# Kernel optimization log

Measured on AMD Instinct MI355X. Metric: run time of the kernel, lower is better.

## Reference

```python
import jax, jax.numpy as jnp
import numpy as np

BINS = 32
MAX_DIST = 128
EMB = 1024
DQ = 64
DV = 64
H = 16
B = 8
L = 1024


def _t5_bucket_table():
    # matches: clamp(n,max=m) + (log(clamp(n,min=m)-m+1)*(bins-1-m)/log(max_distance-m+1)).long()
    n = np.arange(MAX_DIST + 1)
    m = BINS // 2
    idx = np.minimum(n, m) + (
        np.log(np.maximum(n, m) - m + 1) * (BINS - 1 - m) / np.log(MAX_DIST - m + 1)
    ).astype(np.int64)
    return jnp.asarray(idx)


def setup_inputs() -> dict:
    key = jax.random.key(0)
    ks = jax.random.split(key, 8)
    s = 0.02
    return {
        "x": jax.random.normal(ks[0], (B, L, EMB), dtype=jnp.float32),
        "qk_w": jax.random.normal(ks[1], (2 * DQ * H, EMB), dtype=jnp.float32) * s,
        "qk_b": jnp.zeros((2 * DQ * H,), dtype=jnp.float32),
        "v_w": jax.random.normal(ks[2], (DV * H, EMB), dtype=jnp.float32) * s,
        "v_b": jnp.zeros((DV * H,), dtype=jnp.float32),
        "out_w": jax.random.normal(ks[3], (EMB, DV * H), dtype=jnp.float32) * s,
        "out_b": jnp.zeros((EMB,), dtype=jnp.float32),
        "bias": jax.random.normal(ks[4], (BINS, H), dtype=jnp.float32) * s,  # causal -> bins rows
    }


def reference(x, qk_w, qk_b, v_w, v_b, out_w, out_b, bias):
    # projections
    qk = (x @ qk_w.T + qk_b).reshape(B, L, H, 2 * DQ).transpose(0, 2, 1, 3)  # [B,H,L,2DQ]
    q, k = qk[..., :DQ], qk[..., DQ:]
    v = (x @ v_w.T + v_b).reshape(B, L, H, DV).transpose(0, 2, 1, 3)  # [B,H,L,DV]

    # T5 relative-position bias (causal): gather per (i-j) distance bucket
    idx_tab = _t5_bucket_table()
    shifts = jnp.arange(L)[:, None] - jnp.arange(L)[None, :]  # [L,L], i - j
    bins_idx = idx_tab[jnp.clip(jnp.abs(shifts), 0, MAX_DIST)]  # [L,L]
    bmat = bias[bins_idx].transpose(2, 0, 1)  # [H,L,L]
    bmat = jnp.where(shifts < 0, -jnp.inf, bmat)  # causal mask (j > i)

    scale = 1.0 / np.sqrt(DQ).astype(np.float32)
    scores = jnp.einsum("bhid,bhjd->bhij", q, k) * scale + bmat  # [B,H,L,L]
    attn = jax.nn.softmax(scores, axis=-1)
    out = jnp.einsum("bhij,bhjd->bhid", attn, v)  # [B,H,L,DV]
    out = out.transpose(0, 2, 1, 3).reshape(B, L, H * DV)
    return out @ out_w.T + out_b
```

## Files before the change

kernel.cpp:

```cpp
#include <hip/hip_runtime.h>
#include <cmath>


typedef _Float16 f16x8 __attribute__((ext_vector_type(8)));
typedef _Float16 f16x4 __attribute__((ext_vector_type(4)));
typedef float    f32x4 __attribute__((ext_vector_type(4)));

#define NEG_INF (-__builtin_inff())
#define LOG2E 1.4426950408889634f

#if __has_builtin(__builtin_amdgcn_exp2f)
#define EXP2(x) __builtin_amdgcn_exp2f(x)
#else
#define EXP2(x) exp2f(x)
#endif

__device__ __forceinline__ void gl_lds16(const void* g, void* l) {
  __builtin_amdgcn_global_load_lds(
      (__attribute__((address_space(1))) void*)g,
      (__attribute__((address_space(3))) void*)l,
      16, 0, 0);
}

__device__ __forceinline__ f32x4 mfma32(f16x8 a, f16x8 b, f32x4 c) {
  return __builtin_amdgcn_mfma_f32_16x16x32_f16(a, b, c, 0, 0, 0);
}
__device__ __forceinline__ f32x4 mfma16(f16x4 a, f16x4 b, f32x4 c) {
  return __builtin_amdgcn_mfma_f32_16x16x16f16(a, b, c, 0, 0, 0);
}

typedef __attribute__((address_space(3))) _Float16* lds_f16p;

#define DSR(d, a, o) \
  asm volatile("ds_read_b128 %0, %1 offset:" o : "=v"(d) : "v"(a))

__global__ void cvt4_kernel(const float* __restrict__ x,
                            const float* __restrict__ w1,
                            const float* __restrict__ w2,
                            const float* __restrict__ w3,
                            _Float16* __restrict__ ox, _Float16* __restrict__ o1,
                            _Float16* __restrict__ o2, _Float16* __restrict__ o3) {
  const int bid = blockIdx.x;
  const float* src;
  _Float16* dst;
  int idx;
  if (bid < 8192) {
    src = x; dst = ox; idx = bid * 256 + threadIdx.x;
  } else if (bid < 10240) {
    src = w1; dst = o1; idx = (bid - 8192) * 256 + threadIdx.x;
  } else if (bid < 11264) {
    src = w2; dst = o2; idx = (bid - 10240) * 256 + threadIdx.x;
  } else {
    src = w3; dst = o3; idx = (bid - 11264) * 256 + threadIdx.x;
  }
  float4 v = reinterpret_cast<const float4*>(src)[idx];
  f16x4 o;
  o[0] = (_Float16)v.x; o[1] = (_Float16)v.y;
  o[2] = (_Float16)v.z; o[3] = (_Float16)v.w;
  reinterpret_cast<f16x4*>(dst)[idx] = o;
}

#define GEMM_VM8 asm volatile("s_waitcnt vmcnt(8)" ::: "memory")
#define GEMM_VM4 asm volatile("s_waitcnt vmcnt(4)" ::: "memory")
#define GEMM_VM0 asm volatile("s_waitcnt vmcnt(0)" ::: "memory")
#define GEMM_BAR __builtin_amdgcn_s_barrier()

#define GEMM_STAGE(buf, kk)                                        \
  do {                                                             \
    gl_lds16(pA0 + (kk), &lds[(buf)*4096 + wofs]);                 \
    gl_lds16(pA1 + (kk), &lds[(buf)*4096 + 2048 + wofs]);          \
    gl_lds16(pB0 + (kk), &lds[12288 + (buf)*4096 + wofs]);         \
    gl_lds16(pB1 + (kk), &lds[12288 + (buf)*4096 + 2048 + wofs]);  \
  } while (0)

#define GEMM_COMPUTE(aB, bB)                             \
  do {                                                   \
    f16x8 af0, af1, af2, af3, bf0, bf1, bf2, bf3;        \
    DSR(af0, aB, "0");                                   \
    DSR(bf0, bB, "0");                                   \
    DSR(af1, aB, "1024");                                \
    DSR(bf1, bB, "1024");                                \
    DSR(af2, aB, "2048");                                \
    DSR(bf2, bB, "2048");                                \
    DSR(af3, aB, "3072");                                \
    DSR(bf3, bB, "3072");                                \
    asm volatile("s_waitcnt lgkmcnt(4)" ::: "memory");   \
    __builtin_amdgcn_sched_barrier(0);                   \
    __builtin_amdgcn_s_setprio(1);                       \
    acc[0][0] = mfma32(af0, bf0, acc[0][0]);             \
    acc[0][1] = mfma32(af0, bf1, acc[0][1]);             \
    acc[1][0] = mfma32(af1, bf0, acc[1][0]);             \
    acc[1][1] = mfma32(af1, bf1, acc[1][1]);             \
    asm volatile("s_waitcnt lgkmcnt(0)" ::: "memory");   \
    __builtin_amdgcn_sched_barrier(0);                   \
    acc[0][2] = mfma32(af0, bf2, acc[0][2]);             \
    acc[0][3] = mfma32(af0, bf3, acc[0][3]);             \
    acc[1][2] = mfma32(af1, bf2, acc[1][2]);             \
    acc[1][3] = mfma32(af1, bf3, acc[1][3]);             \
    acc[2][0] = mfma32(af2, bf0, acc[2][0]);             \
    acc[2][1] = mfma32(af2, bf1, acc[2][1]);             \
    acc[2][2] = mfma32(af2, bf2, acc[2][2]);             \
    acc[2][3] = mfma32(af2, bf3, acc[2][3]);             \
    acc[3][0] = mfma32(af3, bf0, acc[3][0]);             \
    acc[3][1] = mfma32(af3, bf1, acc[3][1]);             \
    acc[3][2] = mfma32(af3, bf2, acc[3][2]);             \
    acc[3][3] = mfma32(af3, bf3, acc[3][3]);             \
    __builtin_amdgcn_s_setprio(0);                       \
  } while (0)

template <int MODE>
__global__ __launch_bounds__(256, 3) void gemm_kernel(
    const _Float16* __restrict__ A, const _Float16* __restrict__ Bm,
    int M, int N, int K,
    const float* __restrict__ bias_q, const float* __restrict__ bias_v,
    _Float16* __restrict__ qkbuf, _Float16* __restrict__ vtbuf,
    const float* __restrict__ bias_o, float* __restrict__ outf) {
  __shared__ __align__(16) _Float16 lds[6 * 4096];
  const int t = threadIdx.x;
  const int w = t >> 6;
  const int lane = t & 63;
  const int lq = lane & 15, lg = lane >> 4;
  const int wr = w >> 1, wc = w & 1;
  const int m0 = blockIdx.y * 128, n0 = blockIdx.x * 128;

  const int stc = ((t & 3) ^ ((t >> 3) & 3)) * 8;
  const _Float16* pA0 = A + (size_t)(m0 + (t >> 2)) * K + stc;
  const _Float16* pA1 = pA0 + (size_t)64 * K;
  const _Float16* pB0 = Bm + (size_t)(n0 + (t >> 2)) * K + stc;
  const _Float16* pB1 = pB0 + (size_t)64 * K;
  const int wofs = w * 512;

  const int xsw = (lq >> 1) & 3;
  const uint32_t base = (uint32_t)(uintptr_t)(lds_f16p)&lds[0];
  const uint32_t aB0 =
      base + (uint32_t)((wr * 64 + lq) * 64 + ((lg ^ xsw) << 4));
  const uint32_t aB1 = aB0 + 8192;
  const uint32_t aB2 = aB0 + 16384;
  const uint32_t bB0 =
      base + 24576 + (uint32_t)((wc * 64 + lq) * 64 + ((lg ^ xsw) << 4));
  const uint32_t bB1 = bB0 + 8192;
  const uint32_t bB2 = bB0 + 16384;

  f32x4 acc[4][4];
#pragma unroll
  for (int mi = 0; mi < 4; ++mi)
#pragma unroll
    for (int ni = 0; ni < 4; ++ni) acc[mi][ni] = (f32x4){0.f, 0.f, 0.f, 0.f};

  GEMM_STAGE(0, 0);
  GEMM_STAGE(1, 32);
  for (int kt = 0; kt + 160 <= K; kt += 96) {
    GEMM_STAGE(2, kt + 64);
    GEMM_VM8;
    GEMM_BAR;
    GEMM_COMPUTE(aB0, bB0);
    GEMM_BAR;
    GEMM_STAGE(0, kt + 96);
    GEMM_VM8;
    GEMM_BAR;
    GEMM_COMPUTE(aB1, bB1);
    GEMM_BAR;
    GEMM_STAGE(1, kt + 128);
    GEMM_VM8;
    GEMM_BAR;
    GEMM_COMPUTE(aB2, bB2);
    GEMM_BAR;
  }
  GEMM_VM4;
  GEMM_BAR;
  GEMM_COMPUTE(aB0, bB0);
  GEMM_BAR;
  GEMM_VM0;
  GEMM_BAR;
  GEMM_COMPUTE(aB1, bB1);

  if (MODE == 0) {
    GEMM_BAR;
    _Float16* T = &lds[0];
    const bool isqk = (n0 < 2048);
    const int bb = m0 >> 10, ii0 = m0 & 1023;
    if (isqk) {
#pragma unroll
      for (int mi = 0; mi < 4; ++mi)
#pragma unroll
        for (int ni = 0; ni < 4; ++ni) {
          const int col = wc * 64 + ni * 16 + lq;
          const float bq = bias_q[n0 + col];
#pragma unroll
          for (int r = 0; r < 4; ++r) {
            const int row = wr * 64 + mi * 16 + lg * 4 + r;
            T[row * 136 + col] = (_Float16)(acc[mi][ni][r] + bq);
          }
        }
      __syncthreads();
      const int hh = n0 >> 7;
      _Float16* gb = qkbuf + ((size_t)((bb * 16 + hh) * 1024 + ii0)) * 128;
      const int row = t >> 1, half = t & 1;
      const int so = row * 136 + half * 64;
      const int go = row * 128 + half * 64;
#pragma unroll
      for (int j = 0; j < 8; ++j)
        *(f16x8*)(gb + go + j * 8) = *(const f16x8*)&T[so + j * 8];
    } else {
      const int nn0 = n0 - 2048;
#pragma unroll
      for (int mi = 0; mi < 4; ++mi)
#pragma unroll
        for (int ni = 0; ni < 4; ++ni) {
          const int col = wc * 64 + ni * 16 + lq;
          const float bv = bias_v[nn0 + col];
          const int row0 = wr * 64 + mi * 16 + lg * 4;
          f16x4 p;
#pragma unroll
          for (int r = 0; r < 4; ++r) p[r] = (_Float16)(acc[mi][ni][r] + bv);
          *(f16x4*)&T[col * 136 + row0] = p;
        }
      __syncthreads();
      const int c = t >> 1, half = t & 1;
      const int nn = nn0 + c;
      const int hh = nn >> 6, dv = nn & 63;
      _Float16* gb = vtbuf + ((size_t)((bb * 16 + hh) * 64 + dv)) * 1024 +
                     ii0 + half * 64;
      const int so = c * 136 + half * 64;
#pragma unroll
      for (int j = 0; j < 8; ++j)
        *(f16x8*)(gb + j * 8) = *(const f16x8*)&T[so + j * 8];
    }
  } else {
#pragma unroll
    for (int mi = 0; mi < 4; ++mi)
#pragma unroll
      for (int ni = 0; ni < 4; ++ni)
#pragma unroll
        for (int r = 0; r < 4; ++r) {
          const int mg = m0 + wr * 64 + mi * 16 + lg * 4 + r;
          const int ng = n0 + wc * 64 + ni * 16 + lq;
          outf[(size_t)mg * N + ng] = acc[mi][ni][r] + bias_o[ng];
        }
  }
}

__device__ __forceinline__ void stage_kv(const _Float16* __restrict__ kb,
                                         const _Float16* __restrict__ vtb,
                                         int j0, _Float16* kl, _Float16* vl,
                                         int t) {
  const int r0 = t >> 3, c0 = t & 7;
  const int r1 = r0 + 32;
  const int kc0 = c0 ^ (r0 & 7), kc1 = c0 ^ (r1 & 7);
  gl_lds16(kb + (size_t)(j0 + r0) * 128 + kc0 * 8, kl + t * 8);
  gl_lds16(kb + (size_t)(j0 + r1) * 128 + kc1 * 8, kl + (t + 256) * 8);
  gl_lds16(vtb + (size_t)r0 * 1024 + j0 + kc0 * 8, vl + t * 8);
  gl_lds16(vtb + (size_t)r1 * 1024 + j0 + kc1 * 8, vl + (t + 256) * 8);
}

__device__ __forceinline__ void softmax16(f32x4 (&st)[4], f16x4 (&ph)[4],
                                          int qi, int j0, bool far,
                                          const float* __restrict__ tab,
                                          float t128, int lg4, float& m_run,
                                          float& l_part, f32x4 (&oacc)[4]) {
  float xs[16];
  float lmax = NEG_INF;
  if (far) {
#pragma unroll
    for (int js = 0; js < 4; ++js)
#pragma unroll
      for (int r = 0; r < 4; ++r) {
        const float xv = fmaf(st[js][r], 0.125f * LOG2E, t128);
        xs[js * 4 + r] = xv;
        lmax = fmaxf(lmax, xv);
      }
  } else {
#pragma unroll
    for (int js = 0; js < 4; ++js)
#pragma unroll
      for (int r = 0; r < 4; ++r) {
        const int jj = j0 + js * 16 + lg4 + r;
        const int dd = qi - jj;
        const int idx = dd < 0 ? 0 : (dd > 128 ? 128 : dd);
        const float xv =
            (dd < 0) ? NEG_INF : fmaf(st[js][r], 0.125f * LOG2E, tab[idx]);
        xs[js * 4 + r] = xv;
        lmax = fmaxf(lmax, xv);
      }
  }
  if (__any(lmax > m_run + 8.0f)) {
    float tmax = fmaxf(lmax, __shfl_xor(lmax, 16));
    tmax = fmaxf(tmax, __shfl_xor(tmax, 32));
    const float m_new = fmaxf(m_run, tmax);
    const float sf = EXP2(m_run - m_new);
    m_run = m_new;
    l_part *= sf;
    f32x4 sfv;
#pragma unroll
    for (int r = 0; r < 4; ++r) sfv[r] = __shfl(sf, lg4 + r);
#pragma unroll
    for (int db = 0; db < 4; ++db) oacc[db] *= sfv;
  }
  float ls = 0.f;
#pragma unroll
  for (int js = 0; js < 4; ++js)
#pragma unroll
    for (int r = 0; r < 4; ++r) {
      const float p = EXP2(xs[js * 4 + r] - m_run);
      ls += p;
      ph[js][r] = (_Float16)p;
    }
  l_part += ls;
}

__global__ __launch_bounds__(256, 4) void attn_kernel(
    const _Float16* __restrict__ qk,
    const _Float16* __restrict__ vt,
    const float* __restrict__ bias,
    _Float16* __restrict__ ao) {
  __shared__ __align__(16) _Float16 kls[2][64 * 64];
  __shared__ __align__(16) _Float16 vls[2][64 * 64];
  __shared__ float tab[132];
  const int t = threadIdx.x;
  const int bid = blockIdx.x;
  const int bh = (bid & 7) * 16 + (bid >> 6);
  const int b4 = (bid >> 3) & 7;
  const int h = bh & 15, b = bh >> 4;
  if (t < 129) {
    const int bucket =
        (t <= 16) ? t : 16 + (int)(log((double)(t - 15)) * 15.0 / log(113.0));
    tab[t] = bias[bucket * 16 + h] * LOG2E;
  }

  const int w = t >> 6, lane = t & 63;
  const int lq = lane & 15, lg = lane >> 4;
  const int lg4 = lg * 4, lg8 = lg * 8;
  const int tA = b4, tB = 15 - b4;
  const int q0A = tA * 64 + w * 16, q0B = tB * 64 + w * 16;
  const int qA = q0A + lq, qB = q0B + lq;
  const _Float16* qkb = qk + (size_t)bh * 1024 * 128;
  const _Float16* kb = qkb + 64;
  const _Float16* vtb = vt + (size_t)bh * 64 * 1024;

  const f16x8 qfA0 = *(const f16x8*)&qkb[qA * 128 + lg8];
  const f16x8 qfA1 = *(const f16x8*)&qkb[qA * 128 + 32 + lg8];
  const f16x8 qfB0 = *(const f16x8*)&qkb[qB * 128 + lg8];
  const f16x8 qfB1 = *(const f16x8*)&qkb[qB * 128 + 32 + lg8];

  f32x4 oA[4], oB[4];
#pragma unroll
  for (int db = 0; db < 4; ++db) {
    oA[db] = (f32x4){0.f, 0.f, 0.f, 0.f};
    oB[db] = (f32x4){0.f, 0.f, 0.f, 0.f};
  }
  float mA = NEG_INF, lAp = 0.f, mB = NEG_INF, lBp = 0.f;

  stage_kv(kb, vtb, 0, kls[0], vls[0], t);
  __syncthreads();
  const float t128 = tab[128];
  const int krsw = lq & 7;
  const int vsw = (lq & 7) << 1;
  int cur = 0;

  for (int jt = 0; jt <= tB; ++jt) {
    const int j0 = jt * 64;
    if (jt < tB) stage_kv(kb, vtb, j0 + 64, kls[cur ^ 1], vls[cur ^ 1], t);
    const bool aact = (jt <= tA);
    const _Float16* kbf = kls[cur];
    const _Float16* vbf = vls[cur];

    f32x4 stA[4], stB[4];
#pragma unroll
    for (int js = 0; js < 4; ++js) {
      const int rowb = (js * 16 + lq) * 64;
      const f16x8 kf0 = *(const f16x8*)&kbf[rowb + ((lg ^ krsw) << 3)];
      const f16x8 kf1 = *(const f16x8*)&kbf[rowb + (((lg + 4) ^ krsw) << 3)];
      if (aact) {
        stA[js] = mfma32(kf0, qfA0, (f32x4){0.f, 0.f, 0.f, 0.f});
        stA[js] = mfma32(kf1, qfA1, stA[js]);
      }
      stB[js] = mfma32(kf0, qfB0, (f32x4){0.f, 0.f, 0.f, 0.f});
      stB[js] = mfma32(kf1, qfB1, stB[js]);
    }

    f16x4 phA[4], phB[4];
    if (aact)
      softmax16(stA, phA, qA, j0, q0A - j0 >= 192, tab, t128, lg4, mA, lAp,
                oA);
    softmax16(stB, phB, qB, j0, q0B - j0 >= 192, tab, t128, lg4, mB, lBp, oB);

#pragma unroll
    for (int js = 0; js < 4; ++js)
#pragma unroll
      for (int db = 0; db < 4; ++db) {
        const f16x4 vf = *(const f16x4*)&vbf[(db * 16 + lq) * 64 +
                                             ((((js << 2) + lg) ^ vsw) << 2)];
        if (aact) oA[db] = mfma16(phA[js], vf, oA[db]);
        oB[db] = mfma16(phB[js], vf, oB[db]);
      }

    __syncthreads();
    cur ^= 1;
  }

  _Float16* aob = ao + ((size_t)b * 1024) * 1024 + h * 64;
  {
    float lt = lAp + __shfl_xor(lAp, 16);
    lt += __shfl_xor(lt, 32);
    f32x4 linv;
#pragma unroll
    for (int r = 0; r < 4; ++r) linv[r] = 1.0f / __shfl(lt, lg4 + r);
#pragma unroll
    for (int db = 0; db < 4; ++db)
#pragma unroll
      for (int r = 0; r < 4; ++r)
        aob[(size_t)(q0A + lg4 + r) * 1024 + db * 16 + lq] =
            (_Float16)(oA[db][r] * linv[r]);
  }
  {
    float lt = lBp + __shfl_xor(lBp, 16);
    lt += __shfl_xor(lt, 32);
    f32x4 linv;
#pragma unroll
    for (int r = 0; r < 4; ++r) linv[r] = 1.0f / __shfl(lt, lg4 + r);
#pragma unroll
    for (int db = 0; db < 4; ++db)
#pragma unroll
      for (int r = 0; r < 4; ++r)
        aob[(size_t)(q0B + lg4 + r) * 1024 + db * 16 + lq] =
            (_Float16)(oB[db][r] * linv[r]);
  }
}

extern "C" void kernel_launch(void* const* d_in, const int* in_sizes, int n_in,
                              void* d_out, int out_size, void* d_ws,
                              size_t ws_size, hipStream_t stream) {
  const float* x = (const float*)d_in[0];
  const float* qk_w = (const float*)d_in[1];
  const float* qk_b = (const float*)d_in[2];
  const float* v_w = (const float*)d_in[3];
  const float* v_b = (const float*)d_in[4];
  const float* out_w = (const float*)d_in[5];
  const float* out_b = (const float*)d_in[6];
  const float* bias = (const float*)d_in[7];
  float* out = (float*)d_out;

  _Float16* xb = (_Float16*)d_ws;
  _Float16* wb = xb + (size_t)8388608;
  _Float16* owb = wb + (size_t)3145728;
  _Float16* qkbuf = owb + (size_t)1048576;
  _Float16* vtbuf = qkbuf + (size_t)16777216;
  _Float16* ao = vtbuf + (size_t)8388608;

  cvt4_kernel<<<12288, 256, 0, stream>>>(x, qk_w, v_w, out_w, xb, wb,
                                         wb + 2097152, owb);

  gemm_kernel<0><<<dim3(24, 64), 256, 0, stream>>>(
      xb, wb, 8192, 3072, 1024, qk_b, v_b, qkbuf, vtbuf, nullptr, nullptr);

  attn_kernel<<<1024, 256, 0, stream>>>(qkbuf, vtbuf, bias, ao);

  gemm_kernel<1><<<dim3(8, 64), 256, 0, stream>>>(
      ao, owb, 8192, 1024, 1024, nullptr, nullptr, nullptr, nullptr, out_b, out);
}
```

Measured before the change: 157.6 us.

## Share K/V tiles across two query-tile pairs with 512-thread attention blocks

The attention kernel now uses 512-thread blocks, each processing two pairs of causal query tiles. The two pairs share every staged K/V tile, which halves the global-to-LDS staging per query and the block count. Rows whose causal range ends early are masked per wave with a new bact flag, so those waves sit idle on later iterations. Separately, the GEMM main loop is restructured to use a single wait-plus-barrier per stage instead of two barriers, and its loop bound is hardcoded to K=1024.

```diff
diff --git a/kernel.cpp b/kernel.cpp
--- a/kernel.cpp
+++ b/kernel.cpp
@@ -60,7 +60,6 @@
   reinterpret_cast<f16x4*>(dst)[idx] = o;
 }
 
-#define GEMM_VM8 asm volatile("s_waitcnt vmcnt(8)" ::: "memory")
 #define GEMM_VM4 asm volatile("s_waitcnt vmcnt(4)" ::: "memory")
 #define GEMM_VM0 asm volatile("s_waitcnt vmcnt(0)" ::: "memory")
 #define GEMM_BAR __builtin_amdgcn_s_barrier()
@@ -149,27 +148,23 @@
 
   GEMM_STAGE(0, 0);
   GEMM_STAGE(1, 32);
-  for (int kt = 0; kt + 160 <= K; kt += 96) {
+  for (int kt = 0; kt < 960; kt += 96) {
+    GEMM_VM4;
+    GEMM_BAR;
     GEMM_STAGE(2, kt + 64);
-    GEMM_VM8;
-    GEMM_BAR;
     GEMM_COMPUTE(aB0, bB0);
+    GEMM_VM4;
     GEMM_BAR;
     GEMM_STAGE(0, kt + 96);
-    GEMM_VM8;
-    GEMM_BAR;
     GEMM_COMPUTE(aB1, bB1);
+    GEMM_VM4;
     GEMM_BAR;
     GEMM_STAGE(1, kt + 128);
-    GEMM_VM8;
-    GEMM_BAR;
     GEMM_COMPUTE(aB2, bB2);
-    GEMM_BAR;
   }
   GEMM_VM4;
   GEMM_BAR;
   GEMM_COMPUTE(aB0, bB0);
-  GEMM_BAR;
   GEMM_VM0;
   GEMM_BAR;
   GEMM_COMPUTE(aB1, bB1);
@@ -240,17 +235,14 @@
   }
 }
 
-__device__ __forceinline__ void stage_kv(const _Float16* __restrict__ kb,
-                                         const _Float16* __restrict__ vtb,
-                                         int j0, _Float16* kl, _Float16* vl,
-                                         int t) {
-  const int r0 = t >> 3, c0 = t & 7;
-  const int r1 = r0 + 32;
-  const int kc0 = c0 ^ (r0 & 7), kc1 = c0 ^ (r1 & 7);
-  gl_lds16(kb + (size_t)(j0 + r0) * 128 + kc0 * 8, kl + t * 8);
-  gl_lds16(kb + (size_t)(j0 + r1) * 128 + kc1 * 8, kl + (t + 256) * 8);
-  gl_lds16(vtb + (size_t)r0 * 1024 + j0 + kc0 * 8, vl + t * 8);
-  gl_lds16(vtb + (size_t)r1 * 1024 + j0 + kc1 * 8, vl + (t + 256) * 8);
+__device__ __forceinline__ void stage_kv512(const _Float16* __restrict__ kb,
+                                            const _Float16* __restrict__ vtb,
+                                            int j0, _Float16* kl,
+                                            _Float16* vl, int t) {
+  const int r = t >> 3, c = t & 7;
+  const int kc = c ^ (r & 7);
+  gl_lds16(kb + (size_t)(j0 + r) * 128 + kc * 8, kl + t * 8);
+  gl_lds16(vtb + (size_t)r * 1024 + j0 + kc * 8, vl + t * 8);
 }
 
 __device__ __forceinline__ void softmax16(f32x4 (&st)[4], f16x4 (&ph)[4],
@@ -308,7 +300,7 @@
   l_part += ls;
 }
 
-__global__ __launch_bounds__(256, 4) void attn_kernel(
+__global__ __launch_bounds__(512, 4) void attn_kernel(
     const _Float16* __restrict__ qk,
     const _Float16* __restrict__ vt,
     const float* __restrict__ bias,
@@ -318,8 +310,8 @@
   __shared__ float tab[132];
   const int t = threadIdx.x;
   const int bid = blockIdx.x;
-  const int bh = (bid & 7) * 16 + (bid >> 6);
-  const int b4 = (bid >> 3) & 7;
+  const int bh = (bid & 7) * 16 + (bid >> 5);
+  const int q = (bid >> 3) & 3;
   const int h = bh & 15, b = bh >> 4;
   if (t < 129) {
     const int bucket =
@@ -330,8 +322,11 @@
   const int w = t >> 6, lane = t & 63;
   const int lq = lane & 15, lg = lane >> 4;
   const int lg4 = lg * 4, lg8 = lg * 8;
-  const int tA = b4, tB = 15 - b4;
-  const int q0A = tA * 64 + w * 16, q0B = tB * 64 + w * 16;
+  const int pair = w >> 2, wsub = w & 3;
+  const int tA = 2 * q + pair;
+  const int tB = 15 - 2 * q - pair;
+  const int njt = 16 - 2 * q;
+  const int q0A = tA * 64 + wsub * 16, q0B = tB * 64 + wsub * 16;
   const int qA = q0A + lq, qB = q0B + lq;
   const _Float16* qkb = qk + (size_t)bh * 1024 * 128;
   const _Float16* kb = qkb + 64;
@@ -350,17 +345,19 @@
   }
   float mA = NEG_INF, lAp = 0.f, mB = NEG_INF, lBp = 0.f;
 
-  stage_kv(kb, vtb, 0, kls[0], vls[0], t);
+  stage_kv512(kb, vtb, 0, kls[0], vls[0], t);
   __syncthreads();
   const float t128 = tab[128];
   const int krsw = lq & 7;
   const int vsw = (lq & 7) << 1;
   int cur = 0;
 
-  for (int jt = 0; jt <= tB; ++jt) {
+  for (int jt = 0; jt < njt; ++jt) {
     const int j0 = jt * 64;
-    if (jt < tB) stage_kv(kb, vtb, j0 + 64, kls[cur ^ 1], vls[cur ^ 1], t);
+    if (jt + 1 < njt)
+      stage_kv512(kb, vtb, j0 + 64, kls[cur ^ 1], vls[cur ^ 1], t);
     const bool aact = (jt <= tA);
+    const bool bact = (jt <= tB);
     const _Float16* kbf = kls[cur];
     const _Float16* vbf = vls[cur];
 
@@ -374,15 +371,19 @@
         stA[js] = mfma32(kf0, qfA0, (f32x4){0.f, 0.f, 0.f, 0.f});
         stA[js] = mfma32(kf1, qfA1, stA[js]);
       }
-      stB[js] = mfma32(kf0, qfB0, (f32x4){0.f, 0.f, 0.f, 0.f});
-      stB[js] = mfma32(kf1, qfB1, stB[js]);
+      if (bact) {
+        stB[js] = mfma32(kf0, qfB0, (f32x4){0.f, 0.f, 0.f, 0.f});
+        stB[js] = mfma32(kf1, qfB1, stB[js]);
+      }
     }
 
     f16x4 phA[4], phB[4];
     if (aact)
       softmax16(stA, phA, qA, j0, q0A - j0 >= 192, tab, t128, lg4, mA, lAp,
                 oA);
-    softmax16(stB, phB, qB, j0, q0B - j0 >= 192, tab, t128, lg4, mB, lBp, oB);
+    if (bact)
+      softmax16(stB, phB, qB, j0, q0B - j0 >= 192, tab, t128, lg4, mB, lBp,
+                oB);
 
 #pragma unroll
     for (int js = 0; js < 4; ++js)
@@ -391,7 +392,7 @@
         const f16x4 vf = *(const f16x4*)&vbf[(db * 16 + lq) * 64 +
                                              ((((js << 2) + lg) ^ vsw) << 2)];
         if (aact) oA[db] = mfma16(phA[js], vf, oA[db]);
-        oB[db] = mfma16(phB[js], vf, oB[db]);
+        if (bact) oB[db] = mfma16(phB[js], vf, oB[db]);
       }
 
     __syncthreads();
@@ -453,7 +454,7 @@
   gemm_kernel<0><<<dim3(24, 64), 256, 0, stream>>>(
       xb, wb, 8192, 3072, 1024, qk_b, v_b, qkbuf, vtbuf, nullptr, nullptr);
 
-  attn_kernel<<<1024, 256, 0, stream>>>(qkbuf, vtbuf, bias, ao);
+  attn_kernel<<<512, 512, 0, stream>>>(qkbuf, vtbuf, bias, ao);
 
   gemm_kernel<1><<<dim3(8, 64), 256, 0, stream>>>(
       ao, owb, 8192, 1024, 1024, nullptr, nullptr, nullptr, nullptr, out_b, out);
```

Result: slower. 170.1 us (+8.0%).

## Enlarge GEMM tile to 256x128 with 512 threads and single-barrier pipeline

Applied to the files above, without the earlier changes.

The projection GEMMs now use 8 waves per block computing a 256x128 output tile, so each staged B tile is shared by twice as many rows. Each stage issues three async global-to-LDS loads per thread instead of four. The triple-buffered loop is restructured to wait and barrier once before each stage, dropping the trailing barrier after each compute. The V-transpose epilogue is adapted to the wider tile. LDS use grows to 72KB per block, which may limit occupancy. The K loop bound is hardcoded to 960, which assumes K=1024.

```diff
diff --git a/kernel.cpp b/kernel.cpp
--- a/kernel.cpp
+++ b/kernel.cpp
@@ -60,17 +60,15 @@
   reinterpret_cast<f16x4*>(dst)[idx] = o;
 }
 
-#define GEMM_VM8 asm volatile("s_waitcnt vmcnt(8)" ::: "memory")
-#define GEMM_VM4 asm volatile("s_waitcnt vmcnt(4)" ::: "memory")
+#define GEMM_VM3 asm volatile("s_waitcnt vmcnt(3)" ::: "memory")
 #define GEMM_VM0 asm volatile("s_waitcnt vmcnt(0)" ::: "memory")
 #define GEMM_BAR __builtin_amdgcn_s_barrier()
 
-#define GEMM_STAGE(buf, kk)                                        \
-  do {                                                             \
-    gl_lds16(pA0 + (kk), &lds[(buf)*4096 + wofs]);                 \
-    gl_lds16(pA1 + (kk), &lds[(buf)*4096 + 2048 + wofs]);          \
-    gl_lds16(pB0 + (kk), &lds[12288 + (buf)*4096 + wofs]);         \
-    gl_lds16(pB1 + (kk), &lds[12288 + (buf)*4096 + 2048 + wofs]);  \
+#define GEMM_STAGE(buf, kk)                                   \
+  do {                                                        \
+    gl_lds16(pA0 + (kk), &lds[(buf)*8192 + wof]);             \
+    gl_lds16(pA1 + (kk), &lds[(buf)*8192 + 4096 + wof]);      \
+    gl_lds16(pB0 + (kk), &lds[24576 + (buf)*4096 + wof]);     \
   } while (0)
 
 #define GEMM_COMPUTE(aB, bB)                             \
@@ -109,35 +107,34 @@
   } while (0)
 
 template <int MODE>
-__global__ __launch_bounds__(256, 3) void gemm_kernel(
+__global__ __launch_bounds__(512, 4) void gemm_kernel(
     const _Float16* __restrict__ A, const _Float16* __restrict__ Bm,
     int M, int N, int K,
     const float* __restrict__ bias_q, const float* __restrict__ bias_v,
     _Float16* __restrict__ qkbuf, _Float16* __restrict__ vtbuf,
     const float* __restrict__ bias_o, float* __restrict__ outf) {
-  __shared__ __align__(16) _Float16 lds[6 * 4096];
+  __shared__ __align__(16) _Float16 lds[36864];
   const int t = threadIdx.x;
   const int w = t >> 6;
   const int lane = t & 63;
   const int lq = lane & 15, lg = lane >> 4;
   const int wr = w >> 1, wc = w & 1;
-  const int m0 = blockIdx.y * 128, n0 = blockIdx.x * 128;
+  const int m0 = blockIdx.y * 256, n0 = blockIdx.x * 128;
 
   const int stc = ((t & 3) ^ ((t >> 3) & 3)) * 8;
   const _Float16* pA0 = A + (size_t)(m0 + (t >> 2)) * K + stc;
-  const _Float16* pA1 = pA0 + (size_t)64 * K;
+  const _Float16* pA1 = pA0 + (size_t)128 * K;
   const _Float16* pB0 = Bm + (size_t)(n0 + (t >> 2)) * K + stc;
-  const _Float16* pB1 = pB0 + (size_t)64 * K;
-  const int wofs = w * 512;
+  const int wof = w * 512;
 
   const int xsw = (lq >> 1) & 3;
   const uint32_t base = (uint32_t)(uintptr_t)(lds_f16p)&lds[0];
   const uint32_t aB0 =
       base + (uint32_t)((wr * 64 + lq) * 64 + ((lg ^ xsw) << 4));
-  const uint32_t aB1 = aB0 + 8192;
-  const uint32_t aB2 = aB0 + 16384;
+  const uint32_t aB1 = aB0 + 16384;
+  const uint32_t aB2 = aB0 + 32768;
   const uint32_t bB0 =
-      base + 24576 + (uint32_t)((wc * 64 + lq) * 64 + ((lg ^ xsw) << 4));
+      base + 49152 + (uint32_t)((wc * 64 + lq) * 64 + ((lg ^ xsw) << 4));
   const uint32_t bB1 = bB0 + 8192;
   const uint32_t bB2 = bB0 + 16384;
 
@@ -149,27 +146,23 @@
 
   GEMM_STAGE(0, 0);
   GEMM_STAGE(1, 32);
-  for (int kt = 0; kt + 160 <= K; kt += 96) {
+  for (int kt = 0; kt < 960; kt += 96) {
+    GEMM_VM3;
+    GEMM_BAR;
     GEMM_STAGE(2, kt + 64);
-    GEMM_VM8;
-    GEMM_BAR;
     GEMM_COMPUTE(aB0, bB0);
+    GEMM_VM3;
     GEMM_BAR;
     GEMM_STAGE(0, kt + 96);
-    GEMM_VM8;
-    GEMM_BAR;
     GEMM_COMPUTE(aB1, bB1);
+    GEMM_VM3;
     GEMM_BAR;
     GEMM_STAGE(1, kt + 128);
-    GEMM_VM8;
-    GEMM_BAR;
     GEMM_COMPUTE(aB2, bB2);
-    GEMM_BAR;
-  }
-  GEMM_VM4;
+  }
+  GEMM_VM3;
   GEMM_BAR;
   GEMM_COMPUTE(aB0, bB0);
-  GEMM_BAR;
   GEMM_VM0;
   GEMM_BAR;
   GEMM_COMPUTE(aB1, bB1);
@@ -213,15 +206,15 @@
           f16x4 p;
 #pragma unroll
           for (int r = 0; r < 4; ++r) p[r] = (_Float16)(acc[mi][ni][r] + bv);
-          *(f16x4*)&T[col * 136 + row0] = p;
+          *(f16x4*)&T[col * 264 + row0] = p;
         }
       __syncthreads();
-      const int c = t >> 1, half = t & 1;
+      const int c = t >> 2, qd = t & 3;
       const int nn = nn0 + c;
       const int hh = nn >> 6, dv = nn & 63;
       _Float16* gb = vtbuf + ((size_t)((bb * 16 + hh) * 64 + dv)) * 1024 +
-                     ii0 + half * 64;
-      const int so = c * 136 + half * 64;
+                     ii0 + qd * 64;
+      const int so = c * 264 + qd * 64;
 #pragma unroll
       for (int j = 0; j < 8; ++j)
         *(f16x8*)(gb + j * 8) = *(const f16x8*)&T[so + j * 8];
@@ -450,11 +443,11 @@
   cvt4_kernel<<<12288, 256, 0, stream>>>(x, qk_w, v_w, out_w, xb, wb,
                                          wb + 2097152, owb);
 
-  gemm_kernel<0><<<dim3(24, 64), 256, 0, stream>>>(
+  gemm_kernel<0><<<dim3(24, 32), 512, 0, stream>>>(
       xb, wb, 8192, 3072, 1024, qk_b, v_b, qkbuf, vtbuf, nullptr, nullptr);
 
   attn_kernel<<<1024, 256, 0, stream>>>(qkbuf, vtbuf, bias, ao);
 
-  gemm_kernel<1><<<dim3(8, 64), 256, 0, stream>>>(
+  gemm_kernel<1><<<dim3(8, 32), 512, 0, stream>>>(
       ao, owb, 8192, 1024, 1024, nullptr, nullptr, nullptr, nullptr, out_b, out);
 }
```

Result: slower. 160.7 us (+2.0%).

## Use 256x256-tile 8-wave GEMM for fused QKV projection

Applied to the files above, without the earlier changes.

Replaces the 128x128 tile QKV projection GEMM with a new 512-thread kernel computing 256x256 tiles, with each wave holding an 8x4 MFMA accumulator block. It double-buffers K=64 chunks in 128KB of LDS. The larger tile raises arithmetic intensity and cuts global/LDS traffic per FLOP. The epilogue writes through LDS in two 128-column halves. The trade-off is fewer blocks (384 vs 1536), lower occupancy and heavy register pressure. The output projection GEMM is specialised with constant K and N.

```diff
diff --git a/kernel.cpp b/kernel.cpp
--- a/kernel.cpp
+++ b/kernel.cpp
@@ -33,6 +33,11 @@
 
 #define DSR(d, a, o) \
   asm volatile("ds_read_b128 %0, %1 offset:" o : "=v"(d) : "v"(a))
+#define LGKM0SB                                        \
+  asm volatile("s_waitcnt lgkmcnt(0)" ::: "memory");   \
+  __builtin_amdgcn_sched_barrier(0)
+#define VMW(n) asm volatile("s_waitcnt vmcnt(" #n ")" ::: "memory")
+#define SBAR __builtin_amdgcn_s_barrier()
 
 __global__ void cvt4_kernel(const float* __restrict__ x,
                             const float* __restrict__ w1,
@@ -58,6 +63,203 @@
   o[0] = (_Float16)v.x; o[1] = (_Float16)v.y;
   o[2] = (_Float16)v.z; o[3] = (_Float16)v.w;
   reinterpret_cast<f16x4*>(dst)[idx] = o;
+}
+
+#define G8_STA(buf, kh, kk)                                                  \
+  do {                                                                       \
+    gl_lds16(pA + (kk) + (kh) * 32,                                          \
+             &lds[(buf) * 16384 + (kh) * 8192 + wof]);                       \
+    gl_lds16(pA + (kk) + (kh) * 32 + 131072,                                 \
+             &lds[(buf) * 16384 + (kh) * 8192 + 4096 + wof]);                \
+  } while (0)
+#define G8_STB(buf, kh, kk)                                                  \
+  do {                                                                       \
+    gl_lds16(pB + (kk) + (kh) * 32,                                          \
+             &lds[32768 + (buf) * 16384 + (kh) * 8192 + wof]);               \
+    gl_lds16(pB + (kk) + (kh) * 32 + 131072,                                 \
+             &lds[32768 + (buf) * 16384 + (kh) * 8192 + 4096 + wof]);        \
+  } while (0)
+
+#define G8_RDA0                 \
+  do {                          \
+    DSR(aF[0], aK, "0");        \
+    DSR(aF[1], aK, "1024");     \
+    DSR(aF[2], aK, "2048");     \
+    DSR(aF[3], aK, "3072");     \
+    DSR(aF[4], aK, "4096");     \
+    DSR(aF[5], aK, "5120");     \
+    DSR(aF[6], aK, "6144");     \
+    DSR(aF[7], aK, "7168");     \
+  } while (0)
+#define G8_RDA1                 \
+  do {                          \
+    DSR(aF[0], aK, "16384");    \
+    DSR(aF[1], aK, "17408");    \
+    DSR(aF[2], aK, "18432");    \
+    DSR(aF[3], aK, "19456");    \
+    DSR(aF[4], aK, "20480");    \
+    DSR(aF[5], aK, "21504");    \
+    DSR(aF[6], aK, "22528");    \
+    DSR(aF[7], aK, "23552");    \
+  } while (0)
+#define G8_RDB0                 \
+  do {                          \
+    DSR(bF[0], bK, "0");        \
+    DSR(bF[1], bK, "1024");     \
+    DSR(bF[2], bK, "2048");     \
+    DSR(bF[3], bK, "3072");     \
+  } while (0)
+#define G8_RDB1                 \
+  do {                          \
+    DSR(bF[0], bK, "16384");    \
+    DSR(bF[1], bK, "17408");    \
+    DSR(bF[2], bK, "18432");    \
+    DSR(bF[3], bK, "19456");    \
+  } while (0)
+
+#define G8_MM                                                    \
+  do {                                                           \
+    __builtin_amdgcn_s_setprio(1);                               \
+    _Pragma("unroll") for (int mi = 0; mi < 8; ++mi)             \
+        _Pragma("unroll") for (int ni = 0; ni < 4; ++ni)         \
+            acc[mi][ni] = mfma32(aF[mi], bF[ni], acc[mi][ni]);   \
+    __builtin_amdgcn_s_setprio(0);                               \
+  } while (0)
+
+__global__ __launch_bounds__(512, 2) void gemm8_kernel(
+    const _Float16* __restrict__ A, const _Float16* __restrict__ Bm,
+    const float* __restrict__ bias_q, const float* __restrict__ bias_v,
+    _Float16* __restrict__ qkbuf, _Float16* __restrict__ vtbuf) {
+  __shared__ __align__(16) _Float16 lds[65536];
+  const int t = threadIdx.x;
+  const int w = t >> 6, lane = t & 63;
+  const int lq = lane & 15, lg = lane >> 4;
+  const int wm = w >> 2, wn = w & 3;
+  const int m0 = blockIdx.y * 256, n0 = blockIdx.x * 256;
+
+  const int stc = ((t & 3) ^ ((t >> 3) & 3)) * 8;
+  const _Float16* pA = A + (size_t)(m0 + (t >> 2)) * 1024 + stc;
+  const _Float16* pB = Bm + (size_t)(n0 + (t >> 2)) * 1024 + stc;
+  const int wof = w * 512;
+
+  const int xsw = (lq >> 1) & 3;
+  const uint32_t lbase = (uint32_t)(uintptr_t)(lds_f16p)&lds[0];
+  uint32_t aK = lbase + (uint32_t)((wm * 128 + lq) * 64 + ((lg ^ xsw) << 4));
+  uint32_t bK =
+      lbase + 65536u + (uint32_t)((wn * 64 + lq) * 64 + ((lg ^ xsw) << 4));
+
+  f32x4 acc[8][4];
+#pragma unroll
+  for (int mi = 0; mi < 8; ++mi)
+#pragma unroll
+    for (int ni = 0; ni < 4; ++ni) acc[mi][ni] = (f32x4){0.f, 0.f, 0.f, 0.f};
+  f16x8 aF[8], bF[4];
+
+  G8_STA(0, 0, 0);
+  G8_STB(0, 0, 0);
+  G8_STA(0, 1, 0);
+  G8_STB(0, 1, 0);
+
+  int sb = 1;
+  for (int tt = 0; tt < 15; ++tt) {
+    const int kk = (tt + 1) * 64;
+    VMW(4);
+    SBAR;
+    G8_STA(sb, 0, kk);
+    G8_STB(sb, 0, kk);
+    G8_RDA0;
+    G8_RDB0;
+    LGKM0SB;
+    G8_MM;
+    VMW(4);
+    SBAR;
+    G8_STA(sb, 1, kk);
+    G8_STB(sb, 1, kk);
+    G8_RDA1;
+    G8_RDB1;
+    LGKM0SB;
+    G8_MM;
+    aK ^= 32768u;
+    bK ^= 32768u;
+    sb ^= 1;
+  }
+  VMW(4);
+  SBAR;
+  G8_RDA0;
+  G8_RDB0;
+  LGKM0SB;
+  G8_MM;
+  VMW(0);
+  SBAR;
+  G8_RDA1;
+  G8_RDB1;
+  LGKM0SB;
+  G8_MM;
+
+  __syncthreads();
+  _Float16* T = &lds[0];
+  const bool isqk = (n0 < 2048);
+  const int bb = m0 >> 10, ii0 = m0 & 1023;
+  if (isqk) {
+#pragma unroll
+    for (int ch = 0; ch < 2; ++ch) {
+      if ((wn >> 1) == ch) {
+#pragma unroll
+        for (int mi = 0; mi < 8; ++mi)
+#pragma unroll
+          for (int ni = 0; ni < 4; ++ni) {
+            const int col = (wn & 1) * 64 + ni * 16 + lq;
+            const float bq = bias_q[n0 + ch * 128 + col];
+#pragma unroll
+            for (int r = 0; r < 4; ++r) {
+              const int row = wm * 128 + mi * 16 + lg * 4 + r;
+              T[row * 136 + col] = (_Float16)(acc[mi][ni][r] + bq);
+            }
+          }
+      }
+      __syncthreads();
+      const int hh = (n0 >> 7) + ch;
+      _Float16* gb = qkbuf + ((size_t)((bb * 16 + hh) * 1024 + ii0)) * 128;
+      const int row = t >> 1, half = t & 1;
+      const int so = row * 136 + half * 64;
+      const int go = row * 128 + half * 64;
+#pragma unroll
+      for (int j = 0; j < 8; ++j)
+        *(f16x8*)(gb + go + j * 8) = *(const f16x8*)&T[so + j * 8];
+      __syncthreads();
+    }
+  } else {
+    const int nn0 = n0 - 2048;
+#pragma unroll
+    for (int ch = 0; ch < 2; ++ch) {
+      if ((wn >> 1) == ch) {
+#pragma unroll
+        for (int mi = 0; mi < 8; ++mi)
+#pragma unroll
+          for (int ni = 0; ni < 4; ++ni) {
+            const int col = (wn & 1) * 64 + ni * 16 + lq;
+            const float bv = bias_v[nn0 + ch * 128 + col];
+            const int row0 = wm * 128 + mi * 16 + lg * 4;
+            f16x4 p;
+#pragma unroll
+            for (int r = 0; r < 4; ++r)
+              p[r] = (_Float16)(acc[mi][ni][r] + bv);
+            *(f16x4*)&T[col * 264 + row0] = p;
+          }
+      }
+      __syncthreads();
+      const int c = t >> 2, qd = t & 3;
+      const int nn = nn0 + ch * 128 + c;
+      const int hh = nn >> 6, dv = nn & 63;
+      _Float16* gb = vtbuf + ((size_t)((bb * 16 + hh) * 64 + dv)) * 1024 +
+                     ii0 + qd * 64;
+      const int so = c * 264 + qd * 64;
+#pragma unroll
+      for (int j = 0; j < 8; ++j)
+        *(f16x8*)(gb + j * 8) = *(const f16x8*)&T[so + j * 8];
+      __syncthreads();
+    }
+  }
 }
 
 #define GEMM_VM8 asm volatile("s_waitcnt vmcnt(8)" ::: "memory")
@@ -108,13 +310,10 @@
     __builtin_amdgcn_s_setprio(0);                       \
   } while (0)
 
-template <int MODE>
-__global__ __launch_bounds__(256, 3) void gemm_kernel(
+__global__ __launch_bounds__(256, 3) void gemm128_kernel(
     const _Float16* __restrict__ A, const _Float16* __restrict__ Bm,
-    int M, int N, int K,
-    const float* __restrict__ bias_q, const float* __restrict__ bias_v,
-    _Float16* __restrict__ qkbuf, _Float16* __restrict__ vtbuf,
     const float* __restrict__ bias_o, float* __restrict__ outf) {
+  const int K = 1024, N = 1024;
   __shared__ __align__(16) _Float16 lds[6 * 4096];
   const int t = threadIdx.x;
   const int w = t >> 6;
@@ -149,7 +348,7 @@
 
   GEMM_STAGE(0, 0);
   GEMM_STAGE(1, 32);
-  for (int kt = 0; kt + 160 <= K; kt += 96) {
+  for (int kt = 0; kt < 960; kt += 96) {
     GEMM_STAGE(2, kt + 64);
     GEMM_VM8;
     GEMM_BAR;
@@ -174,70 +373,16 @@
   GEMM_BAR;
   GEMM_COMPUTE(aB1, bB1);
 
-  if (MODE == 0) {
-    GEMM_BAR;
-    _Float16* T = &lds[0];
-    const bool isqk = (n0 < 2048);
-    const int bb = m0 >> 10, ii0 = m0 & 1023;
-    if (isqk) {
-#pragma unroll
-      for (int mi = 0; mi < 4; ++mi)
-#pragma unroll
-        for (int ni = 0; ni < 4; ++ni) {
-          const int col = wc * 64 + ni * 16 + lq;
-          const float bq = bias_q[n0 + col];
-#pragma unroll
-          for (int r = 0; r < 4; ++r) {
-            const int row = wr * 64 + mi * 16 + lg * 4 + r;
-            T[row * 136 + col] = (_Float16)(acc[mi][ni][r] + bq);
-          }
-        }
-      __syncthreads();
-      const int hh = n0 >> 7;
-      _Float16* gb = qkbuf + ((size_t)((bb * 16 + hh) * 1024 + ii0)) * 128;
-      const int row = t >> 1, half = t & 1;
-      const int so = row * 136 + half * 64;
-      const int go = row * 128 + half * 64;
-#pragma unroll
-      for (int j = 0; j < 8; ++j)
-        *(f16x8*)(gb + go + j * 8) = *(const f16x8*)&T[so + j * 8];
-    } else {
-      const int nn0 = n0 - 2048;
-#pragma unroll
-      for (int mi = 0; mi < 4; ++mi)
-#pragma unroll
-        for (int ni = 0; ni < 4; ++ni) {
-          const int col = wc * 64 + ni * 16 + lq;
-          const float bv = bias_v[nn0 + col];
-          const int row0 = wr * 64 + mi * 16 + lg * 4;
-          f16x4 p;
-#pragma unroll
-          for (int r = 0; r < 4; ++r) p[r] = (_Float16)(acc[mi][ni][r] + bv);
-          *(f16x4*)&T[col * 136 + row0] = p;
-        }
-      __syncthreads();
-      const int c = t >> 1, half = t & 1;
-      const int nn = nn0 + c;
-      const int hh = nn >> 6, dv = nn & 63;
-      _Float16* gb = vtbuf + ((size_t)((bb * 16 + hh) * 64 + dv)) * 1024 +
-                     ii0 + half * 64;
-      const int so = c * 136 + half * 64;
-#pragma unroll
-      for (int j = 0; j < 8; ++j)
-        *(f16x8*)(gb + j * 8) = *(const f16x8*)&T[so + j * 8];
-    }
-  } else {
-#pragma unroll
-    for (int mi = 0; mi < 4; ++mi)
-#pragma unroll
-      for (int ni = 0; ni < 4; ++ni)
-#pragma unroll
-        for (int r = 0; r < 4; ++r) {
-          const int mg = m0 + wr * 64 + mi * 16 + lg * 4 + r;
-          const int ng = n0 + wc * 64 + ni * 16 + lq;
-          outf[(size_t)mg * N + ng] = acc[mi][ni][r] + bias_o[ng];
-        }
-  }
+#pragma unroll
+  for (int mi = 0; mi < 4; ++mi)
+#pragma unroll
+    for (int ni = 0; ni < 4; ++ni)
+#pragma unroll
+      for (int r = 0; r < 4; ++r) {
+        const int mg = m0 + wr * 64 + mi * 16 + lg * 4 + r;
+        const int ng = n0 + wc * 64 + ni * 16 + lq;
+        outf[(size_t)mg * N + ng] = acc[mi][ni][r] + bias_o[ng];
+      }
 }
 
 __device__ __forceinline__ void stage_kv(const _Float16* __restrict__ kb,
@@ -450,11 +595,10 @@
   cvt4_kernel<<<12288, 256, 0, stream>>>(x, qk_w, v_w, out_w, xb, wb,
                                          wb + 2097152, owb);
 
-  gemm_kernel<0><<<dim3(24, 64), 256, 0, stream>>>(
-      xb, wb, 8192, 3072, 1024, qk_b, v_b, qkbuf, vtbuf, nullptr, nullptr);
+  gemm8_kernel<<<dim3(12, 32), 512, 0, stream>>>(xb, wb, qk_b, v_b, qkbuf,
+                                                 vtbuf);
 
   attn_kernel<<<1024, 256, 0, stream>>>(qkbuf, vtbuf, bias, ao);
 
-  gemm_kernel<1><<<dim3(8, 64), 256, 0, stream>>>(
-      ao, owb, 8192, 1024, 1024, nullptr, nullptr, nullptr, nullptr, out_b, out);
-}
+  gemm128_kernel<<<dim3(8, 64), 256, 0, stream>>>(ao, owb, out_b, out);
+}
```

Result: slower. 163.7 us (+3.9%).
